# Optimization experiments

Hardware: AMD Instinct MI355X
Metric: run time of the kernel (lower is better)

Reference implementation:

```python
import jax, jax.numpy as jnp
import numpy as np

B, T, S, H = 32, 1, 4096, 1024

def setup_inputs() -> dict:
    key = jax.random.key(0)
    ks = jax.random.split(key, 8)
    query = jax.random.normal(ks[0], (B, T, H), dtype=jnp.float32)
    encoder_outputs = jax.random.normal(ks[1], (B, S, H), dtype=jnp.float32)
    src_lengths = jax.random.randint(ks[2], (B,), 1, S + 1, dtype=jnp.int64)
    sc = 1.0 / np.sqrt(H)
    Ws_w = jax.random.normal(ks[3], (H, H), dtype=jnp.float32) * sc   # torch Linear weight (out,in)
    Wh_w = jax.random.normal(ks[4], (H, H), dtype=jnp.float32) * sc
    v_w = jax.random.normal(ks[5], (1, H), dtype=jnp.float32) * sc
    Wout_w = jax.random.normal(ks[6], (H, 2 * H), dtype=jnp.float32) * sc
    return {"query": query, "encoder_outputs": encoder_outputs, "src_lengths": src_lengths,
            "Ws_w": Ws_w, "Wh_w": Wh_w, "v_w": v_w, "Wout_w": Wout_w}

def reference(query, encoder_outputs, src_lengths, Ws_w, Wh_w, v_w, Wout_w):
    # score(h, s) = v^T tanh(Ws q + Wh h); query is a single decoder step (T=1)
    q_proj = jnp.einsum('bth,oh->bto', query, Ws_w)            # (B,1,H)
    h_proj = jnp.einsum('bsh,oh->bso', encoder_outputs, Wh_w)  # (B,S,H)
    scores = jnp.einsum('bsh,h->bs', jnp.tanh(q_proj + h_proj), v_w[0])  # (B,S)
    # NOTE: original calls non-in-place masked_fill and discards the result,
    # so src_lengths has no effect on the output (replicated faithfully).
    attn = jax.nn.softmax(scores, axis=-1)                     # (B,S)
    ctx = jnp.einsum('bs,bsh->bh', attn, encoder_outputs)[:, None, :]  # (B,1,H)
    cat = jnp.concatenate([ctx, query], axis=-1)               # (B,1,2H)
    return jnp.tanh(jnp.einsum('btk,ok->bto', cat, Wout_w))    # (B,1,H)
```

## Files before the change

kernel.cpp:

```cpp
#include <hip/hip_runtime.h>
#include <hip/hip_bf16.h>

#define B_  32
#define S_  4096
#define H_  1024
#define M_  (B_*S_)

typedef __attribute__((ext_vector_type(8))) short bf16x8;
typedef __attribute__((ext_vector_type(4))) float f32x4;
typedef __attribute__((ext_vector_type(8))) unsigned short ushort8;

typedef void __attribute__((address_space(3)))* lds_ptr_t;
typedef void __attribute__((address_space(1)))* gbl_ptr_t;

__device__ __forceinline__ unsigned short f2bf(float x) {
    return __builtin_bit_cast(unsigned short, __float2bfloat16(x));
}
__device__ __forceinline__ float bf2f(unsigned short u) {
    return __builtin_bit_cast(float, (unsigned)u << 16);
}
__device__ __forceinline__ float tanh_fast(float x) {
    float e = __expf(2.0f * x);
    return 1.0f - 2.0f / (e + 1.0f);
}

__global__ __launch_bounds__(256) void k_cvt_bf16(const float* __restrict__ in,
                                                  unsigned short* __restrict__ out, int n4) {
    int i = blockIdx.x * 256 + threadIdx.x;
    if (i < n4) {
        float4 f = reinterpret_cast<const float4*>(in)[i];
        ushort4 u;
        u.x = f2bf(f.x); u.y = f2bf(f.y); u.z = f2bf(f.z); u.w = f2bf(f.w);
        reinterpret_cast<ushort4*>(out)[i] = u;
    }
}

__global__ __launch_bounds__(256) void k_cvt_enc(const float* __restrict__ in,
                                                 unsigned short* __restrict__ out, int n8) {
    const int stride = gridDim.x * 256;
    for (int i = blockIdx.x * 256 + threadIdx.x; i < n8; i += stride) {
        float4 a = reinterpret_cast<const float4*>(in)[(size_t)i * 2];
        float4 b = reinterpret_cast<const float4*>(in)[(size_t)i * 2 + 1];
        ushort8 u;
        u[0] = f2bf(a.x); u[1] = f2bf(a.y); u[2] = f2bf(a.z); u[3] = f2bf(a.w);
        u[4] = f2bf(b.x); u[5] = f2bf(b.y); u[6] = f2bf(b.z); u[7] = f2bf(b.w);
        reinterpret_cast<ushort8*>(out)[i] = u;
    }
}

__global__ __launch_bounds__(256) void k_qproj(const float* __restrict__ q,
                                               const float* __restrict__ Ws,
                                               float* __restrict__ qp) {
    const int b = blockIdx.y, oc = blockIdx.x, tid = threadIdx.x;
    __shared__ float ql[H_];
    for (int i = tid; i < H_; i += 256) ql[i] = q[b*H_ + i];
    __syncthreads();
    const int o = oc*256 + tid;
    const float4* w = reinterpret_cast<const float4*>(&Ws[(size_t)o * H_]);
    float acc = 0.f;
    #pragma unroll 4
    for (int k4 = 0; k4 < H_/4; ++k4) {
        float4 ww = w[k4];
        acc += ql[k4*4+0]*ww.x + ql[k4*4+1]*ww.y + ql[k4*4+2]*ww.z + ql[k4*4+3]*ww.w;
    }
    qp[b*H_ + o] = acc;
}

__global__ __launch_bounds__(256) void k_scores_b(const unsigned short* __restrict__ encb,
                                                  const unsigned short* __restrict__ whb,
                                                  const float* __restrict__ qp,
                                                  const float* __restrict__ vw,
                                                  float* __restrict__ sp) {
    __shared__ __align__(16) unsigned short As[2][128][32];
    __shared__ __align__(16) unsigned short Bs[2][128][32];
    __shared__ float sred[2][128];

    const int tid  = threadIdx.x;
    const int lane = tid & 63;
    const int wid  = tid >> 6;
    const int wr = wid >> 1, wc = wid & 1;
    const int fr = lane & 15;
    const int fk = (lane >> 4) * 8;

    const int h  = blockIdx.x;
    const int L  = (h & 7) * 1024 + (h >> 3);
    const int bm = L >> 3;
    const int bn = L & 7;
    const int row0 = bm * 128;
    const int col0 = bn * 128;
    const int b = row0 >> 12;

    const int sr = tid >> 2;
    const int sk = (tid & 3) * 8;

    auto stage = [&](int buf, int kt) {
        const unsigned short* ga0 = encb + (size_t)(row0 + sr) * H_ + kt*32 + sk;
        const unsigned short* gb0 = whb  + (size_t)(col0 + sr) * H_ + kt*32 + sk;
        char* la = (char*)(&As[buf][0][0]) + tid*16;
        char* lb = (char*)(&Bs[buf][0][0]) + tid*16;
        __builtin_amdgcn_global_load_lds((gbl_ptr_t)ga0,                 (lds_ptr_t)la,        16, 0, 0);
        __builtin_amdgcn_global_load_lds((gbl_ptr_t)(ga0 + (size_t)64*H_),(lds_ptr_t)(la+4096), 16, 0, 0);
        __builtin_amdgcn_global_load_lds((gbl_ptr_t)gb0,                 (lds_ptr_t)lb,        16, 0, 0);
        __builtin_amdgcn_global_load_lds((gbl_ptr_t)(gb0 + (size_t)64*H_),(lds_ptr_t)(lb+4096), 16, 0, 0);
    };

    f32x4 acc[4][4] = {};

    stage(0, 0);
    __syncthreads();

    for (int kt = 0; kt < 32; ++kt) {
        const int cur = kt & 1, nxt = cur ^ 1;
        if (kt < 31) stage(nxt, kt + 1);

        bf16x8 af[4], bfr[4];
        #pragma unroll
        for (int i = 0; i < 4; ++i) {
            af[i]  = *reinterpret_cast<const bf16x8*>(&As[cur][wr*64 + i*16 + fr][fk]);
            bfr[i] = *reinterpret_cast<const bf16x8*>(&Bs[cur][wc*64 + i*16 + fr][fk]);
        }
        #pragma unroll
        for (int i = 0; i < 4; ++i)
            #pragma unroll
            for (int j = 0; j < 4; ++j)
                acc[i][j] = __builtin_amdgcn_mfma_f32_16x16x32_bf16(af[i], bfr[j], acc[i][j], 0, 0, 0);

        __syncthreads();
    }

    float vv[4], qq[4];
    #pragma unroll
    for (int j = 0; j < 4; ++j) {
        int c = col0 + wc*64 + j*16 + fr;
        vv[j] = vw[c];
        qq[j] = qp[b*H_ + c];
    }
    #pragma unroll
    for (int i = 0; i < 4; ++i) {
        #pragma unroll
        for (int r = 0; r < 4; ++r) {
            float s = 0.f;
            #pragma unroll
            for (int j = 0; j < 4; ++j)
                s += vv[j] * tanh_fast(qq[j] + acc[i][j][r]);
            #pragma unroll
            for (int m = 1; m < 16; m <<= 1)
                s += __shfl_xor(s, m, 64);
            if (fr == 0)
                sred[wc][wr*64 + i*16 + (lane >> 4)*4 + r] = s;
        }
    }
    __syncthreads();
    if (tid < 128)
        sp[(size_t)bn * M_ + row0 + tid] = sred[0][tid] + sred[1][tid];
}

__global__ __launch_bounds__(256) void k_scores_f(const float* __restrict__ enc,
                                                  const unsigned short* __restrict__ whb,
                                                  const float* __restrict__ qp,
                                                  const float* __restrict__ vw,
                                                  float* __restrict__ sp) {
    __shared__ __align__(16) unsigned short As[2][128][32];
    __shared__ __align__(16) unsigned short Bs[2][128][32];
    __shared__ float sred[2][128];

    const int tid  = threadIdx.x;
    const int lane = tid & 63;
    const int wid  = tid >> 6;
    const int wr = wid >> 1, wc = wid & 1;
    const int fr = lane & 15;
    const int fk = (lane >> 4) * 8;

    const int h  = blockIdx.x;
    const int L  = (h & 7) * 1024 + (h >> 3);
    const int bm = L >> 3;
    const int bn = L & 7;
    const int row0 = bm * 128;
    const int col0 = bn * 128;
    const int b = row0 >> 12;

    const int ar = tid >> 3;
    const int ak = (tid & 7) * 4;
    const int bnr = tid >> 2;
    const int bkk = (tid & 3) * 8;

    float4 areg[4];
    auto loadA = [&](int kt) {
        #pragma unroll
        for (int p = 0; p < 4; ++p)
            areg[p] = *reinterpret_cast<const float4*>(
                &enc[(size_t)(row0 + p*32 + ar) * H_ + kt*32 + ak]);
    };
    auto writeA = [&](int buf) {
        #pragma unroll
        for (int p = 0; p < 4; ++p) {
            ushort4 u;
            u.x = f2bf(areg[p].x); u.y = f2bf(areg[p].y);
            u.z = f2bf(areg[p].z); u.w = f2bf(areg[p].w);
            *reinterpret_cast<ushort4*>(&As[buf][p*32 + ar][ak]) = u;
        }
    };
    auto stageB = [&](int buf, int kt) {
        const unsigned short* g0 = whb + (size_t)(col0 + bnr) * H_ + kt*32 + bkk;
        const unsigned short* g1 = g0 + (size_t)64 * H_;
        char* l0 = (char*)(&Bs[buf][0][0]) + tid*16;
        __builtin_amdgcn_global_load_lds((gbl_ptr_t)g0, (lds_ptr_t)l0,        16, 0, 0);
        __builtin_amdgcn_global_load_lds((gbl_ptr_t)g1, (lds_ptr_t)(l0+4096), 16, 0, 0);
    };

    f32x4 acc[4][4] = {};

    loadA(0);
    stageB(0, 0);
    writeA(0);
    __syncthreads();

    for (int kt = 0; kt < 32; ++kt) {
        const int cur = kt & 1, nxt = cur ^ 1;
        if (kt < 31) { stageB(nxt, kt + 1); loadA(kt + 1); }

        bf16x8 af[4], bfr[4];
        #pragma unroll
        for (int i = 0; i < 4; ++i) {
            af[i]  = *reinterpret_cast<const bf16x8*>(&As[cur][wr*64 + i*16 + fr][fk]);
            bfr[i] = *reinterpret_cast<const bf16x8*>(&Bs[cur][wc*64 + i*16 + fr][fk]);
        }
        #pragma unroll
        for (int i = 0; i < 4; ++i)
            #pragma unroll
            for (int j = 0; j < 4; ++j)
                acc[i][j] = __builtin_amdgcn_mfma_f32_16x16x32_bf16(af[i], bfr[j], acc[i][j], 0, 0, 0);

        if (kt < 31) writeA(nxt);
        __syncthreads();
    }

    float vv[4], qq[4];
    #pragma unroll
    for (int j = 0; j < 4; ++j) {
        int c = col0 + wc*64 + j*16 + fr;
        vv[j] = vw[c];
        qq[j] = qp[b*H_ + c];
    }
    #pragma unroll
    for (int i = 0; i < 4; ++i) {
        #pragma unroll
        for (int r = 0; r < 4; ++r) {
            float s = 0.f;
            #pragma unroll
            for (int j = 0; j < 4; ++j)
                s += vv[j] * tanh_fast(qq[j] + acc[i][j][r]);
            #pragma unroll
            for (int m = 1; m < 16; m <<= 1)
                s += __shfl_xor(s, m, 64);
            if (fr == 0)
                sred[wc][wr*64 + i*16 + (lane >> 4)*4 + r] = s;
        }
    }
    __syncthreads();
    if (tid < 128)
        sp[(size_t)bn * M_ + row0 + tid] = sred[0][tid] + sred[1][tid];
}

__global__ __launch_bounds__(256) void k_softmax(const float* __restrict__ sp,
                                                 float* __restrict__ attn) {
    const int b = blockIdx.x, tid = threadIdx.x;
    __shared__ float red[4];
    float vals[16];
    float mx = -1e30f;
    #pragma unroll
    for (int i = 0; i < 16; ++i) {
        int s = i*256 + tid;
        float x = 0.f;
        #pragma unroll
        for (int p = 0; p < 8; ++p) x += sp[(size_t)p*M_ + b*S_ + s];
        vals[i] = x;
        mx = fmaxf(mx, x);
    }
    #pragma unroll
    for (int m = 1; m < 64; m <<= 1) mx = fmaxf(mx, __shfl_xor(mx, m, 64));
    if ((tid & 63) == 0) red[tid >> 6] = mx;
    __syncthreads();
    mx = fmaxf(fmaxf(red[0], red[1]), fmaxf(red[2], red[3]));
    float sum = 0.f;
    #pragma unroll
    for (int i = 0; i < 16; ++i) { vals[i] = __expf(vals[i] - mx); sum += vals[i]; }
    #pragma unroll
    for (int m = 1; m < 64; m <<= 1) sum += __shfl_xor(sum, m, 64);
    __syncthreads();
    if ((tid & 63) == 0) red[tid >> 6] = sum;
    __syncthreads();
    sum = red[0] + red[1] + red[2] + red[3];
    float inv = 1.f / sum;
    #pragma unroll
    for (int i = 0; i < 16; ++i) attn[b*S_ + i*256 + tid] = vals[i] * inv;
}

__global__ __launch_bounds__(256) void k_ctx_b(const float* __restrict__ attn,
                                               const unsigned short* __restrict__ encb,
                                               float* __restrict__ ctxp) {
    const int sc = blockIdx.x;
    const int b  = blockIdx.y;
    const int hh = threadIdx.x * 4;
    float ax = 0.f, ay = 0.f, az = 0.f, aw = 0.f;
    const int s0 = sc * 256;
    #pragma unroll 4
    for (int s = s0; s < s0 + 256; ++s) {
        float a = attn[b*S_ + s];
        ushort4 e = *reinterpret_cast<const ushort4*>(&encb[((size_t)b*S_ + s) * H_ + hh]);
        ax += a*bf2f(e.x); ay += a*bf2f(e.y); az += a*bf2f(e.z); aw += a*bf2f(e.w);
    }
    float4 o; o.x = ax; o.y = ay; o.z = az; o.w = aw;
    *reinterpret_cast<float4*>(&ctxp[((size_t)sc*B_ + b) * H_ + hh]) = o;
}

__global__ __launch_bounds__(256) void k_ctx_f(const float* __restrict__ attn,
                                               const float* __restrict__ enc,
                                               float* __restrict__ ctxp) {
    const int sc = blockIdx.x;
    const int b  = blockIdx.y;
    const int hh = threadIdx.x * 4;
    float ax = 0.f, ay = 0.f, az = 0.f, aw = 0.f;
    const int s0 = sc * 256;
    #pragma unroll 4
    for (int s = s0; s < s0 + 256; ++s) {
        float a = attn[b*S_ + s];
        float4 e = *reinterpret_cast<const float4*>(&enc[((size_t)b*S_ + s) * H_ + hh]);
        ax += a*e.x; ay += a*e.y; az += a*e.z; aw += a*e.w;
    }
    float4 o; o.x = ax; o.y = ay; o.z = az; o.w = aw;
    *reinterpret_cast<float4*>(&ctxp[((size_t)sc*B_ + b) * H_ + hh]) = o;
}

__global__ __launch_bounds__(256) void k_out(const float* __restrict__ ctxp,
                                             const float* __restrict__ q,
                                             const float* __restrict__ Wout,
                                             float* __restrict__ out) {
    const int oc = blockIdx.x, b = blockIdx.y, tid = threadIdx.x;
    __shared__ float cat[2*H_];
    for (int k = tid; k < H_; k += 256) {
        float s = 0.f;
        #pragma unroll
        for (int p = 0; p < 16; ++p) s += ctxp[((size_t)p*B_ + b) * H_ + k];
        cat[k] = s;
        cat[H_ + k] = q[b*H_ + k];
    }
    __syncthreads();
    const int o = oc*256 + tid;
    const float4* w = reinterpret_cast<const float4*>(&Wout[(size_t)o * 2*H_]);
    float acc = 0.f;
    #pragma unroll 4
    for (int k4 = 0; k4 < 2*H_/4; ++k4) {
        float4 ww = w[k4];
        acc += cat[k4*4+0]*ww.x + cat[k4*4+1]*ww.y + cat[k4*4+2]*ww.z + cat[k4*4+3]*ww.w;
    }
    out[b*H_ + o] = tanh_fast(acc);
}

extern "C" void kernel_launch(void* const* d_in, const int* in_sizes, int n_in,
                              void* d_out, int out_size, void* d_ws, size_t ws_size,
                              hipStream_t stream) {
    const float* query = (const float*)d_in[0];
    const float* enc   = (const float*)d_in[1];
    const float* Ws    = (const float*)d_in[3];
    const float* Wh    = (const float*)d_in[4];
    const float* vw    = (const float*)d_in[5];
    const float* Wout  = (const float*)d_in[6];
    float* out = (float*)d_out;

    char* ws = (char*)d_ws;

    if (ws_size >= (266ull << 20)) {
        unsigned short* encb = (unsigned short*)ws;
        unsigned short* whb  = (unsigned short*)(ws + (256ull << 20));
        float* sp   = (float*)(ws + (258ull << 20));
        float* attn = (float*)(ws + (262ull << 20));
        float* qp   = (float*)(ws + (262ull << 20) + (512u << 10));
        float* ctxp = (float*)(ws + (263ull << 20));

        k_cvt_enc <<<dim3(2048),    dim3(256), 0, stream>>>(enc, encb, M_*H_/8);
        k_cvt_bf16<<<dim3(1024),    dim3(256), 0, stream>>>(Wh, whb, H_*H_/4);
        k_qproj   <<<dim3(4, 32),   dim3(256), 0, stream>>>(query, Ws, qp);
        k_scores_b<<<dim3(8192),    dim3(256), 0, stream>>>(encb, whb, qp, vw, sp);
        k_softmax <<<dim3(32),      dim3(256), 0, stream>>>(sp, attn);
        k_ctx_b   <<<dim3(16, 32),  dim3(256), 0, stream>>>(attn, encb, ctxp);
        k_out     <<<dim3(4, 32),   dim3(256), 0, stream>>>(ctxp, query, Wout, out);
    } else {
        unsigned short* whb = (unsigned short*)ws;
        float* sp   = (float*)(ws + (2u  << 20));
        float* attn = (float*)(ws + (6u  << 20));
        float* qp   = (float*)(ws + (6u  << 20) + (512u << 10));
        float* ctxp = (float*)(ws + (7u  << 20));

        k_cvt_bf16<<<dim3(1024),    dim3(256), 0, stream>>>(Wh, whb, H_*H_/4);
        k_qproj   <<<dim3(4, 32),   dim3(256), 0, stream>>>(query, Ws, qp);
        k_scores_f<<<dim3(8192),    dim3(256), 0, stream>>>(enc, whb, qp, vw, sp);
        k_softmax <<<dim3(32),      dim3(256), 0, stream>>>(sp, attn);
        k_ctx_f   <<<dim3(16, 32),  dim3(256), 0, stream>>>(attn, enc, ctxp);
        k_out     <<<dim3(4, 32),   dim3(256), 0, stream>>>(ctxp, query, Wout, out);
    }
}
```

Baseline: 672.0 us.

## Replace bf16 score GEMM with 256x256 tiled 8-wave pipelined MFMA kernel

```diff
diff --git a/kernel.cpp b/kernel.cpp
--- a/kernel.cpp
+++ b/kernel.cpp
@@ -66,93 +66,160 @@
     qp[b*H_ + o] = acc;
 }
 
-__global__ __launch_bounds__(256) void k_scores_b(const unsigned short* __restrict__ encb,
-                                                  const unsigned short* __restrict__ whb,
-                                                  const float* __restrict__ qp,
-                                                  const float* __restrict__ vw,
-                                                  float* __restrict__ sp) {
-    __shared__ __align__(16) unsigned short As[2][128][32];
-    __shared__ __align__(16) unsigned short Bs[2][128][32];
-    __shared__ float sred[2][128];
-
-    const int tid  = threadIdx.x;
-    const int lane = tid & 63;
-    const int wid  = tid >> 6;
-    const int wr = wid >> 1, wc = wid & 1;
-    const int fr = lane & 15;
-    const int fk = (lane >> 4) * 8;
-
-    const int h  = blockIdx.x;
-    const int L  = (h & 7) * 1024 + (h >> 3);
-    const int bm = L >> 3;
-    const int bn = L & 7;
-    const int row0 = bm * 128;
-    const int col0 = bn * 128;
+__global__ __launch_bounds__(512, 2) void k_scores8(const unsigned short* __restrict__ encb,
+                                                    const unsigned short* __restrict__ whb,
+                                                    const float* __restrict__ qp,
+                                                    const float* __restrict__ vw,
+                                                    float* __restrict__ sp) {
+    __shared__ __align__(1024) char smem[131072];
+
+    const int tid = threadIdx.x;
+    const int l   = tid & 63;
+    const int w   = tid >> 6;
+    const int wr  = w >> 2;
+    const int wc  = w & 3;
+    const int fr  = l & 15;
+    const int fh  = l >> 4;
+
+    const int hb = blockIdx.x;
+    const int L  = (hb & 7) * 256 + (hb >> 3);
+    const int bm = L >> 2;
+    const int bn = L & 3;
+    const int row0 = bm * 256;
+    const int col0 = bn * 256;
     const int b = row0 >> 12;
 
-    const int sr = tid >> 2;
-    const int sk = (tid & 3) * 8;
-
-    auto stage = [&](int buf, int kt) {
-        const unsigned short* ga0 = encb + (size_t)(row0 + sr) * H_ + kt*32 + sk;
-        const unsigned short* gb0 = whb  + (size_t)(col0 + sr) * H_ + kt*32 + sk;
-        char* la = (char*)(&As[buf][0][0]) + tid*16;
-        char* lb = (char*)(&Bs[buf][0][0]) + tid*16;
-        __builtin_amdgcn_global_load_lds((gbl_ptr_t)ga0,                 (lds_ptr_t)la,        16, 0, 0);
-        __builtin_amdgcn_global_load_lds((gbl_ptr_t)(ga0 + (size_t)64*H_),(lds_ptr_t)(la+4096), 16, 0, 0);
-        __builtin_amdgcn_global_load_lds((gbl_ptr_t)gb0,                 (lds_ptr_t)lb,        16, 0, 0);
-        __builtin_amdgcn_global_load_lds((gbl_ptr_t)(gb0 + (size_t)64*H_),(lds_ptr_t)(lb+4096), 16, 0, 0);
-    };
-
-    f32x4 acc[4][4] = {};
-
-    stage(0, 0);
-    __syncthreads();
-
-    for (int kt = 0; kt < 32; ++kt) {
-        const int cur = kt & 1, nxt = cur ^ 1;
-        if (kt < 31) stage(nxt, kt + 1);
-
-        bf16x8 af[4], bfr[4];
-        #pragma unroll
-        for (int i = 0; i < 4; ++i) {
-            af[i]  = *reinterpret_cast<const bf16x8*>(&As[cur][wr*64 + i*16 + fr][fk]);
-            bfr[i] = *reinterpret_cast<const bf16x8*>(&Bs[cur][wc*64 + i*16 + fr][fk]);
-        }
-        #pragma unroll
-        for (int i = 0; i < 4; ++i)
-            #pragma unroll
-            for (int j = 0; j < 4; ++j)
-                acc[i][j] = __builtin_amdgcn_mfma_f32_16x16x32_bf16(af[i], bfr[j], acc[i][j], 0, 0, 0);
-
-        __syncthreads();
-    }
+    const int srow = l >> 2;
+    const int scol = (l & 3) * 8;
+
+    auto stageA = [&](int t, int mh) {
+        #pragma unroll
+        for (int j = 0; j < 2; ++j) {
+            int s_local = j*8 + w;
+            int g  = s_local >> 1;
+            int kh = s_local & 1;
+            int rblk = mh*4 + (g & 3) + ((g >> 2) << 3);
+            const unsigned short* src = encb + (size_t)(row0 + rblk*16 + srow) * H_
+                                             + t*64 + kh*32 + scol;
+            char* dst = smem + (t & 1)*65536 + (rblk*2 + kh)*1024 + l*16;
+            __builtin_amdgcn_global_load_lds((gbl_ptr_t)src, (lds_ptr_t)dst, 16, 0, 0);
+        }
+    };
+    auto stageB = [&](int t, int q) {
+        #pragma unroll
+        for (int j = 0; j < 2; ++j) {
+            int s_local = j*8 + w;
+            int a2 = s_local >> 2;
+            int b2 = (s_local >> 1) & 1;
+            int kh = s_local & 1;
+            int nblk = a2*4 + q*2 + b2;
+            const unsigned short* src = whb + (size_t)(col0 + nblk*16 + srow) * H_
+                                            + t*64 + kh*32 + scol;
+            char* dst = smem + (t & 1)*65536 + 32768 + (nblk*2 + kh)*1024 + l*16;
+            __builtin_amdgcn_global_load_lds((gbl_ptr_t)src, (lds_ptr_t)dst, 16, 0, 0);
+        }
+    };
+
+    f32x4  acc[8][4] = {};
+    bf16x8 af[4][2];
+    bf16x8 ba[4][2];
+
+    auto ldA = [&](int buf, int mq) {
+        #pragma unroll
+        for (int m2 = 0; m2 < 4; ++m2)
+            #pragma unroll
+            for (int kh = 0; kh < 2; ++kh) {
+                int rblk = wr*8 + mq*4 + m2;
+                af[m2][kh] = *reinterpret_cast<const bf16x8*>(
+                    smem + buf*65536 + (rblk*2 + kh)*1024 + fr*64 + fh*16);
+            }
+    };
+    auto ldB = [&](int buf, int nq) {
+        #pragma unroll
+        for (int n2 = 0; n2 < 2; ++n2)
+            #pragma unroll
+            for (int kh = 0; kh < 2; ++kh) {
+                int nblk = wc*4 + nq*2 + n2;
+                ba[nq*2 + n2][kh] = *reinterpret_cast<const bf16x8*>(
+                    smem + buf*65536 + 32768 + (nblk*2 + kh)*1024 + fr*64 + fh*16);
+            }
+    };
+    auto mfma16 = [&](int mq, int nq) {
+        __builtin_amdgcn_s_setprio(1);
+        #pragma unroll
+        for (int kh = 0; kh < 2; ++kh)
+            #pragma unroll
+            for (int m2 = 0; m2 < 4; ++m2)
+                #pragma unroll
+                for (int n2 = 0; n2 < 2; ++n2)
+                    acc[mq*4+m2][nq*2+n2] = __builtin_amdgcn_mfma_f32_16x16x32_bf16(
+                        af[m2][kh], ba[nq*2+n2][kh], acc[mq*4+m2][nq*2+n2], 0, 0, 0);
+        __builtin_amdgcn_s_setprio(0);
+    };
+
+    auto tile = [&](int t, bool s1, bool s2, bool last) {
+        const int buf = t & 1;
+        ldA(buf, 0); ldB(buf, 0);
+        if (s1) stageA(t+1, 1);
+        __builtin_amdgcn_s_barrier();
+        asm volatile("s_waitcnt lgkmcnt(0)" ::: "memory");
+        mfma16(0, 0);
+        __builtin_amdgcn_s_barrier();
+        ldB(buf, 1);
+        if (s2) stageA(t+2, 0);
+        __builtin_amdgcn_s_barrier();
+        asm volatile("s_waitcnt lgkmcnt(0)" ::: "memory");
+        mfma16(0, 1);
+        __builtin_amdgcn_s_barrier();
+        ldA(buf, 1);
+        if (s2) stageB(t+2, 0);
+        __builtin_amdgcn_s_barrier();
+        asm volatile("s_waitcnt lgkmcnt(0)" ::: "memory");
+        mfma16(1, 0);
+        __builtin_amdgcn_s_barrier();
+        if (s2) stageB(t+2, 1);
+        __builtin_amdgcn_s_barrier();
+        asm volatile("s_waitcnt lgkmcnt(0)" ::: "memory");
+        mfma16(1, 1);
+        if (!last) asm volatile("s_waitcnt vmcnt(6)" ::: "memory");
+        else       asm volatile("s_waitcnt vmcnt(0)" ::: "memory");
+        __builtin_amdgcn_s_barrier();
+    };
+
+    stageA(0, 0); stageB(0, 0); stageB(0, 1); stageA(0, 1);
+    stageA(1, 0); stageB(1, 0); stageB(1, 1);
+    asm volatile("s_waitcnt vmcnt(6)" ::: "memory");
+    __builtin_amdgcn_s_barrier();
+
+    for (int t = 0; t < 14; ++t) tile(t, true, true, false);
+    tile(14, true,  false, true);
+    tile(15, false, false, true);
 
     float vv[4], qq[4];
     #pragma unroll
-    for (int j = 0; j < 4; ++j) {
-        int c = col0 + wc*64 + j*16 + fr;
-        vv[j] = vw[c];
-        qq[j] = qp[b*H_ + c];
-    }
-    #pragma unroll
-    for (int i = 0; i < 4; ++i) {
+    for (int n = 0; n < 4; ++n) {
+        int c = col0 + wc*64 + n*16 + fr;
+        vv[n] = vw[c];
+        qq[n] = qp[b*H_ + c];
+    }
+    float* sred = (float*)smem;
+    #pragma unroll
+    for (int m = 0; m < 8; ++m)
         #pragma unroll
         for (int r = 0; r < 4; ++r) {
             float s = 0.f;
             #pragma unroll
-            for (int j = 0; j < 4; ++j)
-                s += vv[j] * tanh_fast(qq[j] + acc[i][j][r]);
-            #pragma unroll
-            for (int m = 1; m < 16; m <<= 1)
-                s += __shfl_xor(s, m, 64);
-            if (fr == 0)
-                sred[wc][wr*64 + i*16 + (lane >> 4)*4 + r] = s;
-        }
-    }
-    __syncthreads();
-    if (tid < 128)
-        sp[(size_t)bn * M_ + row0 + tid] = sred[0][tid] + sred[1][tid];
+            for (int n = 0; n < 4; ++n)
+                s += vv[n] * tanh_fast(qq[n] + acc[m][n][r]);
+            s += __shfl_xor(s, 1, 64); s += __shfl_xor(s, 2, 64);
+            s += __shfl_xor(s, 4, 64); s += __shfl_xor(s, 8, 64);
+            if (fr == 0) sred[wc*256 + wr*128 + m*16 + fh*4 + r] = s;
+        }
+    __syncthreads();
+    if (tid < 256) {
+        float s = sred[tid] + sred[256 + tid] + sred[512 + tid] + sred[768 + tid];
+        sp[(size_t)bn * M_ + row0 + tid] = s;
+    }
 }
 
 __global__ __launch_bounds__(256) void k_scores_f(const float* __restrict__ enc,
@@ -263,7 +330,7 @@
 }
 
 __global__ __launch_bounds__(256) void k_softmax(const float* __restrict__ sp,
-                                                 float* __restrict__ attn) {
+                                                 float* __restrict__ attn, int P) {
     const int b = blockIdx.x, tid = threadIdx.x;
     __shared__ float red[4];
     float vals[16];
@@ -272,8 +339,7 @@
     for (int i = 0; i < 16; ++i) {
         int s = i*256 + tid;
         float x = 0.f;
-        #pragma unroll
-        for (int p = 0; p < 8; ++p) x += sp[(size_t)p*M_ + b*S_ + s];
+        for (int p = 0; p < P; ++p) x += sp[(size_t)p*M_ + b*S_ + s];
         vals[i] = x;
         mx = fmaxf(mx, x);
     }
@@ -381,8 +447,8 @@
         k_cvt_enc <<<dim3(2048),    dim3(256), 0, stream>>>(enc, encb, M_*H_/8);
         k_cvt_bf16<<<dim3(1024),    dim3(256), 0, stream>>>(Wh, whb, H_*H_/4);
         k_qproj   <<<dim3(4, 32),   dim3(256), 0, stream>>>(query, Ws, qp);
-        k_scores_b<<<dim3(8192),    dim3(256), 0, stream>>>(encb, whb, qp, vw, sp);
-        k_softmax <<<dim3(32),      dim3(256), 0, stream>>>(sp, attn);
+        k_scores8 <<<dim3(2048),    dim3(512), 0, stream>>>(encb, whb, qp, vw, sp);
+        k_softmax <<<dim3(32),      dim3(256), 0, stream>>>(sp, attn, 4);
         k_ctx_b   <<<dim3(16, 32),  dim3(256), 0, stream>>>(attn, encb, ctxp);
         k_out     <<<dim3(4, 32),   dim3(256), 0, stream>>>(ctxp, query, Wout, out);
     } else {
@@ -395,7 +461,7 @@
         k_cvt_bf16<<<dim3(1024),    dim3(256), 0, stream>>>(Wh, whb, H_*H_/4);
         k_qproj   <<<dim3(4, 32),   dim3(256), 0, stream>>>(query, Ws, qp);
         k_scores_f<<<dim3(8192),    dim3(256), 0, stream>>>(enc, whb, qp, vw, sp);
-        k_softmax <<<dim3(32),      dim3(256), 0, stream>>>(sp, attn);
+        k_softmax <<<dim3(32),      dim3(256), 0, stream>>>(sp, attn, 8);
         k_ctx_f   <<<dim3(16, 32),  dim3(256), 0, stream>>>(attn, enc, ctxp);
         k_out     <<<dim3(4, 32),   dim3(256), 0, stream>>>(ctxp, query, Wout, out);
     }
```

Measured after the change: 650.9 us. -3.2%, faster.
